# Kernel optimization log

Hardware: AMD Instinct MI355X
Metric: run time of the kernel (lower is better)

The kernel has to match this reference:

```python
import jax, jax.numpy as jnp
import numpy as np

LN_EPS = 1e-5
N_HEAD_CHANNELS = 32  # model_dim=256 -> 8 heads


def _layer_norm(x, g, b):
    m = jnp.mean(x, axis=-1, keepdims=True)
    v = jnp.mean((x - m) ** 2, axis=-1, keepdims=True)
    return (x - m) * jax.lax.rsqrt(v + LN_EPS) * g + b


def setup_inputs() -> dict:
    key = jax.random.key(0)
    ks = jax.random.split(key, 12)
    b, n, nv, f = 1, 65536, 1, 256
    s = 256  # 4 ** seq_level_attention
    w = 0.02
    d = {}
    d["x"] = jax.random.normal(ks[0], (b, n, nv, f), jnp.float32)
    d["mask"] = jnp.ones((b, n, nv), dtype=bool)
    d["pos_embeddings"] = jax.random.normal(ks[1], (nv, s, f), jnp.float32) * w
    d["W_emb"] = jax.random.normal(ks[2], (f, 2 * f), jnp.float32) * w
    d["b_emb"] = jnp.zeros((2 * f,), jnp.float32)
    d["ln1_g"] = jnp.ones((f,), jnp.float32)
    d["ln1_b"] = jnp.zeros((f,), jnp.float32)
    d["Wq"] = jax.random.normal(ks[3], (f, f), jnp.float32) * w
    d["bq"] = jnp.zeros((f,), jnp.float32)
    d["Wk"] = jax.random.normal(ks[4], (f, f), jnp.float32) * w
    d["bk"] = jnp.zeros((f,), jnp.float32)
    d["Wv"] = jax.random.normal(ks[5], (f, f), jnp.float32) * w
    d["bv"] = jnp.zeros((f,), jnp.float32)
    d["Wo"] = jax.random.normal(ks[6], (f, f), jnp.float32) * w
    d["bo"] = jnp.zeros((f,), jnp.float32)
    d["ln2_g"] = jnp.ones((f,), jnp.float32)
    d["ln2_b"] = jnp.zeros((f,), jnp.float32)
    d["W1"] = jax.random.normal(ks[7], (f, f), jnp.float32) * w
    d["W2"] = jax.random.normal(ks[8], (f, f), jnp.float32) * w
    d["gamma"] = jnp.ones((f,), jnp.float32) * 1e-6
    d["gamma_mlp"] = jnp.ones((f,), jnp.float32) * 1e-6
    return d


def reference(x, mask, pos_embeddings, W_emb, b_emb, ln1_g, ln1_b,
              Wq, bq, Wk, bk, Wv, bv, Wo, bo, ln2_g, ln2_b, W1, W2,
              gamma, gamma_mlp):
    b, n, nv, f = x.shape
    s = pos_embeddings.shape[1]          # window length = 4**seq_level
    n_seq = n // s
    n_heads = f // N_HEAD_CHANNELS
    hd = f // n_heads

    x_res = x
    # sequenize: (b, n, nv, f) -> (b, n_seq, s, nv, f)
    xs = x.reshape(b, n_seq, s, nv, f)
    ms = mask.reshape(b, n_seq, s, nv)
    # mask_update: a vertex stays valid only if its whole window is valid
    mask_update = (ms & jnp.all(ms, axis=-2, keepdims=True)).reshape(b, n, nv)

    # shift/scale from position embeddings: (nv, s, 2f) -> (s, nv, 2f)
    emb = jnp.swapaxes(pos_embeddings @ W_emb + b_emb, -2, -3)
    shift, scale = jnp.split(emb, 2, axis=-1)  # each (s, nv, f)

    xm = _layer_norm(xs, ln1_g, ln1_b) * (scale + 1.0) + shift

    B = b * n_seq
    L = s * nv
    xf = xm.reshape(B, L, f)
    mf = ms.reshape(B, L)

    def heads(t):
        return t.reshape(B, L, n_heads, hd).transpose(0, 2, 1, 3)

    q = heads(xf @ Wq + bq)
    k = heads(xf @ Wk + bk)
    v = heads(xf @ Wv + bv)

    scores = jnp.einsum('bhqd,bhkd->bhqk', q, k) / np.sqrt(hd).astype(np.float32)
    scores = scores + jnp.where(mf[:, None, None, :], 0.0, -1e9)
    attn = jax.nn.softmax(scores, axis=-1)
    out = jnp.einsum('bhqk,bhkd->bhqd', attn, v)
    out = out.transpose(0, 2, 1, 3).reshape(B, L, f) @ Wo + bo

    x = x_res + gamma * out.reshape(b, n, nv, f)
    h = _layer_norm(x, ln2_g, ln2_b) @ W1
    h = jax.nn.silu(h) @ W2
    x = x + gamma_mlp * h
    return (x, mask_update)
```

## Files before the change

kernel.cpp:

```cpp
#include <hip/hip_runtime.h>
#include <cstddef>
#include <cstdint>

typedef unsigned short u16;
typedef short s16x8 __attribute__((ext_vector_type(8)));
typedef float f32x4 __attribute__((ext_vector_type(4)));
typedef int   i32x4 __attribute__((ext_vector_type(4)));
typedef u16   u16x4 __attribute__((ext_vector_type(4)));

__device__ __forceinline__ float b2f(u16 u) {
  union { unsigned int i; float f; } v; v.i = ((unsigned int)u) << 16; return v.f;
}
__device__ __forceinline__ u16 f2b(float f) {
  union { float f; unsigned int i; } v; v.f = f;
  unsigned int r = v.i + 0x7fffu + ((v.i >> 16) & 1u);
  return (u16)(r >> 16);
}
__device__ __forceinline__ unsigned int cvt_pk(float a, float b) {
  unsigned int r;
  asm("v_cvt_pk_bf16_f32 %0, %1, %2" : "=v"(r) : "v"(a), "v"(b));
  return r;
}

__global__ __launch_bounds__(256) void transpose6(
    const float* __restrict__ w0, const float* __restrict__ w1,
    const float* __restrict__ w2, const float* __restrict__ w3,
    const float* __restrict__ w4, const float* __restrict__ w5,
    u16* __restrict__ wt)
{
  __shared__ u16 T[64][66];
  const float* src;
  switch (blockIdx.x) {
    case 0: src = w0; break; case 1: src = w1; break;
    case 2: src = w2; break; case 3: src = w3; break;
    case 4: src = w4; break; default: src = w5; break;
  }
  u16* dst = wt + (size_t)blockIdx.x * 65536;
  const int tr = (blockIdx.y & 3) * 64;
  const int tc = (blockIdx.y >> 2) * 64;
  const int lane = threadIdx.x & 63, grp = threadIdx.x >> 6;
  #pragma unroll
  for (int i = 0; i < 16; ++i) {
    const int r = grp + i * 4;
    T[lane][r] = f2b(src[(size_t)(tr + r) * 256 + tc + lane]);
  }
  __syncthreads();
  #pragma unroll
  for (int i = 0; i < 16; ++i) {
    const int j = grp + i * 4;
    dst[(size_t)(tc + j) * 256 + tr + lane] = T[j][lane];
  }
}

__global__ __launch_bounds__(256) void film_kernel(
    const float* __restrict__ pos, const float* __restrict__ Wemb,
    const float* __restrict__ bemb, float* __restrict__ shift,
    float* __restrict__ scale)
{
  __shared__ float prow[256];
  __shared__ float psum[4][64];
  const int s = blockIdx.x, t = threadIdx.x;
  const int ks = t >> 6, cl = t & 63;
  const int c = blockIdx.y * 64 + cl;
  prow[t] = pos[s * 256 + t];
  __syncthreads();
  float acc = 0.f;
  #pragma unroll 8
  for (int kk = ks * 64; kk < ks * 64 + 64; ++kk)
    acc = fmaf(prow[kk], Wemb[kk * 512 + c], acc);
  psum[ks][cl] = acc;
  __syncthreads();
  if (t < 64) {
    const int cc = blockIdx.y * 64 + t;
    const float v = psum[0][t] + psum[1][t] + psum[2][t] + psum[3][t] + bemb[cc];
    if (cc < 256) shift[s * 256 + cc] = v;
    else          scale[s * 256 + cc - 256] = v;
  }
}

__global__ __launch_bounds__(256) void ln_kernel(
    const float* __restrict__ xf,
    const float* __restrict__ shift, const float* __restrict__ scale,
    const float* __restrict__ g, const float* __restrict__ b,
    u16* __restrict__ out)
{
  const int lane = threadIdx.x & 63;
  const int l = lane & 15, grp = lane >> 4;
  const int token = blockIdx.x * 16 + (threadIdx.x >> 6) * 4 + grp;
  const size_t tb = (size_t)token * 256;
  const int spos = token & 255;

  f32x4 v[4];
  #pragma unroll
  for (int j = 0; j < 4; ++j) v[j] = *(const f32x4*)(xf + tb + 4 * l + 64 * j);
  float s = 0.f, s2 = 0.f;
  #pragma unroll
  for (int j = 0; j < 4; ++j)
    #pragma unroll
    for (int i = 0; i < 4; ++i) { s += v[j][i]; s2 += v[j][i] * v[j][i]; }
  #pragma unroll
  for (int off = 8; off >= 1; off >>= 1) {
    s  += __shfl_xor(s, off);
    s2 += __shfl_xor(s2, off);
  }
  const float mean = s * 0.00390625f;
  const float inv  = rsqrtf(s2 * 0.00390625f - mean * mean + 1e-5f);
  #pragma unroll
  for (int j = 0; j < 4; ++j) {
    const int e = 4 * l + 64 * j;
    const f32x4 gv = *(const f32x4*)(g + e);
    const f32x4 bv = *(const f32x4*)(b + e);
    const f32x4 sc = *(const f32x4*)(scale + spos * 256 + e);
    const f32x4 sh = *(const f32x4*)(shift + spos * 256 + e);
    u16x4 o;
    #pragma unroll
    for (int i = 0; i < 4; ++i) {
      float ln = (v[j][i] - mean) * inv * gv[i] + bv[i];
      ln = ln * (sc[i] + 1.0f) + sh[i];
      o[i] = f2b(ln);
    }
    *(u16x4*)(out + tb + e) = o;
  }
}

__global__ __launch_bounds__(256) void gemm_qkv(
    const u16* __restrict__ A, const u16* __restrict__ wt,
    const float* __restrict__ bq, const float* __restrict__ bk,
    const float* __restrict__ bv, u16* __restrict__ qo,
    u16* __restrict__ ko, u16* __restrict__ vo)
{
  __shared__ __align__(16) u16 Alds[128][72];
  __shared__ __align__(16) u16 Blds[128][72];
  const int bid = blockIdx.x;
  const int xcd = bid & 7, rr = bid >> 3;
  const int xx = rr % 6;
  const int yy = (rr / 6) * 8 + xcd;
  const int wsel = xx >> 1;
  const int m0 = yy * 128;
  const int n0 = (xx & 1) * 128;
  const u16* BT = wt + (size_t)wsel * 65536;
  const int t = threadIdx.x;
  const int wave = t >> 6, lane = t & 63;
  const int wm = (wave & 1) * 64, wn = (wave >> 1) * 64;
  const int lrow = lane & 15, lk = (lane >> 4) * 8;

  f32x4 acc[4][4];
  #pragma unroll
  for (int i = 0; i < 4; ++i)
    #pragma unroll
    for (int j = 0; j < 4; ++j)
      acc[i][j] = f32x4{0.f, 0.f, 0.f, 0.f};

  for (int k0 = 0; k0 < 256; k0 += 64) {
    #pragma unroll
    for (int i = 0; i < 4; ++i) {
      const int c = i * 256 + t;
      const int row = c >> 3, col = (c & 7) * 8;
      *(i32x4*)(&Alds[row][col]) = *(const i32x4*)(A  + (size_t)(m0 + row) * 256 + k0 + col);
      *(i32x4*)(&Blds[row][col]) = *(const i32x4*)(BT + (size_t)(n0 + row) * 256 + k0 + col);
    }
    __syncthreads();
    #pragma unroll
    for (int kk = 0; kk < 64; kk += 32) {
      s16x8 af[4], bf[4];
      #pragma unroll
      for (int mt = 0; mt < 4; ++mt) af[mt] = *(const s16x8*)(&Alds[wm + mt*16 + lrow][kk + lk]);
      #pragma unroll
      for (int nt = 0; nt < 4; ++nt) bf[nt] = *(const s16x8*)(&Blds[wn + nt*16 + lrow][kk + lk]);
      #pragma unroll
      for (int mt = 0; mt < 4; ++mt)
        #pragma unroll
        for (int nt = 0; nt < 4; ++nt)
          acc[mt][nt] = __builtin_amdgcn_mfma_f32_16x16x32_bf16(af[mt], bf[nt], acc[mt][nt], 0, 0, 0);
    }
    __syncthreads();
  }

  const float* bias = (wsel == 0) ? bq : (wsel == 1) ? bk : bv;
  u16* qko = (wsel == 0) ? qo : ko;
  #pragma unroll
  for (int mt = 0; mt < 4; ++mt) {
    const int mb = m0 + wm + mt*16 + (lane >> 4) * 4;
    const int w = mb >> 8, tok = mb & 255;
    #pragma unroll
    for (int nt = 0; nt < 4; ++nt) {
      const int n = n0 + wn + nt*16 + lrow;
      const int h = n >> 5, d = n & 31;
      const float bv_ = bias[n];
      if (wsel < 2) {
        #pragma unroll
        for (int r = 0; r < 4; ++r)
          qko[(size_t)w * 65536 + h * 8192 + (tok + r) * 32 + d] = f2b(acc[mt][nt][r] + bv_);
      } else {
        u16x4 pk;
        #pragma unroll
        for (int r = 0; r < 4; ++r) pk[r] = f2b(acc[mt][nt][r] + bv_);
        const int vaddr = ((tok >> 5) << 10) + (((tok >> 2) & 3) << 8)
                        + d * 8 + (((tok >> 4) & 1) << 2);
        *(u16x4*)(vo + (size_t)w * 65536 + h * 8192 + vaddr) = pk;
      }
    }
  }
}

__global__ __launch_bounds__(512) void gemm_tail(
    const u16* __restrict__ A, const u16* __restrict__ WoT,
    const u16* __restrict__ W1T, const u16* __restrict__ W2T,
    const float* __restrict__ bo, const float* __restrict__ x,
    const float* __restrict__ gam, const float* __restrict__ lg2,
    const float* __restrict__ lb2, const float* __restrict__ gml,
    float* __restrict__ outx)
{
  __shared__ __align__(16) u16 XH[64][264];
  __shared__ float LNp[4][64][2];
  __shared__ float LNm[64][2];
  const int m0 = blockIdx.x * 64;
  const int t = threadIdx.x;
  const int wave = t >> 6, lane = t & 63;
  const int wm = (wave & 1) * 32, wn = (wave >> 1) * 64;
  const int lrow = lane & 15, lk = (lane >> 4) * 8;
  const int quad = lane >> 4, col = lane & 15;

  f32x4 acc[2][4];
  #pragma unroll
  for (int i = 0; i < 2; ++i)
    #pragma unroll
    for (int j = 0; j < 4; ++j) acc[i][j] = f32x4{0.f,0.f,0.f,0.f};

  #pragma unroll 2
  for (int k0 = 0; k0 < 256; k0 += 32) {
    s16x8 af[2], bf[4];
    #pragma unroll
    for (int mt = 0; mt < 2; ++mt)
      af[mt] = *(const s16x8*)(A + (size_t)(m0 + wm + mt*16 + lrow) * 256 + k0 + lk);
    #pragma unroll
    for (int nt = 0; nt < 4; ++nt)
      bf[nt] = *(const s16x8*)(WoT + (size_t)(wn + nt*16 + lrow) * 256 + k0 + lk);
    #pragma unroll
    for (int mt = 0; mt < 2; ++mt)
      #pragma unroll
      for (int nt = 0; nt < 4; ++nt)
        acc[mt][nt] = __builtin_amdgcn_mfma_f32_16x16x32_bf16(af[mt], bf[nt], acc[mt][nt], 0, 0, 0);
  }

  unsigned int x1p[2][4][2];
  float s[2][4], s2[2][4];
  #pragma unroll
  for (int mt = 0; mt < 2; ++mt)
    #pragma unroll
    for (int r = 0; r < 4; ++r) { s[mt][r] = 0.f; s2[mt][r] = 0.f; }

  #pragma unroll
  for (int mt = 0; mt < 2; ++mt) {
    const int mb = m0 + wm + mt*16 + quad*4;
    #pragma unroll
    for (int nt = 0; nt < 4; ++nt) {
      const int n = wn + nt*16 + col;
      const float bon = bo[n], gn = gam[n];
      float v[4];
      #pragma unroll
      for (int r = 0; r < 4; ++r)
        v[r] = x[(size_t)(mb + r) * 256 + n] + gn * (acc[mt][nt][r] + bon);
      const unsigned int p0 = cvt_pk(v[0], v[1]);
      const unsigned int p1 = cvt_pk(v[2], v[3]);
      x1p[mt][nt][0] = p0;
      x1p[mt][nt][1] = p1;
      const float r0 = b2f((u16)(p0 & 0xffffu)), r1 = b2f((u16)(p0 >> 16));
      const float r2 = b2f((u16)(p1 & 0xffffu)), r3 = b2f((u16)(p1 >> 16));
      s[mt][0] += r0; s2[mt][0] += r0 * r0;
      s[mt][1] += r1; s2[mt][1] += r1 * r1;
      s[mt][2] += r2; s2[mt][2] += r2 * r2;
      s[mt][3] += r3; s2[mt][3] += r3 * r3;
    }
  }
  #pragma unroll
  for (int off = 1; off <= 8; off <<= 1) {
    #pragma unroll
    for (int mt = 0; mt < 2; ++mt)
      #pragma unroll
      for (int r = 0; r < 4; ++r) {
        s[mt][r]  += __shfl_xor(s[mt][r],  off);
        s2[mt][r] += __shfl_xor(s2[mt][r], off);
      }
  }
  if (col == 0) {
    #pragma unroll
    for (int mt = 0; mt < 2; ++mt)
      #pragma unroll
      for (int r = 0; r < 4; ++r) {
        const int row = wm + mt*16 + quad*4 + r;
        LNp[wave >> 1][row][0] = s[mt][r];
        LNp[wave >> 1][row][1] = s2[mt][r];
      }
  }
  __syncthreads();
  if (t < 64) {
    const float ss  = LNp[0][t][0] + LNp[1][t][0] + LNp[2][t][0] + LNp[3][t][0];
    const float ss2 = LNp[0][t][1] + LNp[1][t][1] + LNp[2][t][1] + LNp[3][t][1];
    const float mean = ss * 0.00390625f;
    LNm[t][0] = mean;
    LNm[t][1] = rsqrtf(ss2 * 0.00390625f - mean * mean + 1e-5f);
  }
  __syncthreads();
  #pragma unroll
  for (int mt = 0; mt < 2; ++mt) {
    #pragma unroll
    for (int nt = 0; nt < 4; ++nt) {
      const int n = wn + nt*16 + col;
      const float gg = lg2[n], bb_ = lb2[n];
      #pragma unroll
      for (int rr = 0; rr < 2; ++rr) {
        const unsigned int pk = x1p[mt][nt][rr];
        #pragma unroll
        for (int h2 = 0; h2 < 2; ++h2) {
          const int r = rr * 2 + h2;
          const int row = wm + mt*16 + quad*4 + r;
          const float rv = b2f((u16)(h2 ? (pk >> 16) : (pk & 0xffffu)));
          const float xn = (rv - LNm[row][0]) * LNm[row][1] * gg + bb_;
          XH[row][n ^ ((row & 12) << 1)] = f2b(xn);
        }
      }
    }
  }
  __syncthreads();

  #pragma unroll
  for (int i = 0; i < 2; ++i)
    #pragma unroll
    for (int j = 0; j < 4; ++j) acc[i][j] = f32x4{0.f,0.f,0.f,0.f};
  #pragma unroll 2
  for (int k0 = 0; k0 < 256; k0 += 32) {
    s16x8 af[2], bf[4];
    #pragma unroll
    for (int mt = 0; mt < 2; ++mt) {
      const int row = wm + mt*16 + lrow;
      af[mt] = *(const s16x8*)(&XH[row][(k0 + lk) ^ ((row & 12) << 1)]);
    }
    #pragma unroll
    for (int nt = 0; nt < 4; ++nt)
      bf[nt] = *(const s16x8*)(W1T + (size_t)(wn + nt*16 + lrow) * 256 + k0 + lk);
    #pragma unroll
    for (int mt = 0; mt < 2; ++mt)
      #pragma unroll
      for (int nt = 0; nt < 4; ++nt)
        acc[mt][nt] = __builtin_amdgcn_mfma_f32_16x16x32_bf16(af[mt], bf[nt], acc[mt][nt], 0, 0, 0);
  }
  __syncthreads();
  #pragma unroll
  for (int mt = 0; mt < 2; ++mt)
    #pragma unroll
    for (int nt = 0; nt < 4; ++nt)
      #pragma unroll
      for (int r = 0; r < 4; ++r) {
        const float y = acc[mt][nt][r];
        const float hsig = __builtin_amdgcn_rcpf(1.0f + __builtin_amdgcn_exp2f(-1.442695041f * y));
        const int row = wm + mt*16 + quad*4 + r;
        const int n = wn + nt*16 + col;
        XH[row][n ^ ((row & 12) << 1)] = f2b(y * hsig);
        acc[mt][nt][r] = 0.0f;
      }
  __syncthreads();

  #pragma unroll 2
  for (int k0 = 0; k0 < 256; k0 += 32) {
    s16x8 af[2], bf[4];
    #pragma unroll
    for (int mt = 0; mt < 2; ++mt) {
      const int row = wm + mt*16 + lrow;
      af[mt] = *(const s16x8*)(&XH[row][(k0 + lk) ^ ((row & 12) << 1)]);
    }
    #pragma unroll
    for (int nt = 0; nt < 4; ++nt)
      bf[nt] = *(const s16x8*)(W2T + (size_t)(wn + nt*16 + lrow) * 256 + k0 + lk);
    #pragma unroll
    for (int mt = 0; mt < 2; ++mt)
      #pragma unroll
      for (int nt = 0; nt < 4; ++nt)
        acc[mt][nt] = __builtin_amdgcn_mfma_f32_16x16x32_bf16(af[mt], bf[nt], acc[mt][nt], 0, 0, 0);
  }

  #pragma unroll
  for (int mt = 0; mt < 2; ++mt) {
    const int mb = m0 + wm + mt*16 + quad*4;
    #pragma unroll
    for (int nt = 0; nt < 4; ++nt) {
      const int n = wn + nt*16 + col;
      const float gn = gml[n];
      #pragma unroll
      for (int rr = 0; rr < 2; ++rr) {
        const unsigned int pk = x1p[mt][nt][rr];
        outx[(size_t)(mb + rr*2    ) * 256 + n] = b2f((u16)(pk & 0xffffu)) + gn * acc[mt][nt][rr*2];
        outx[(size_t)(mb + rr*2 + 1) * 256 + n] = b2f((u16)(pk >> 16))     + gn * acc[mt][nt][rr*2 + 1];
      }
    }
  }
}

__global__ __launch_bounds__(512) void attn256(
    const u16* __restrict__ q, const u16* __restrict__ k,
    const u16* __restrict__ vt, const float* __restrict__ fbias,
    u16* __restrict__ out)
{
  __shared__ __align__(16) u16 KV[16384];
  __shared__ __align__(16) u16 OB[8][16][40];
  const int bid = blockIdx.x;
  const int xcd = bid & 7, rr = bid >> 3;
  const int q0 = (rr & 1) * 128;
  const int s_ = (rr >> 1) * 8 + xcd;
  const int h = s_ & 7, w = s_ >> 3;
  const int t = threadIdx.x;
  const int wave = t >> 6, lane = t & 63;
  const int col = lane & 15, quad = lane >> 4;
  const size_t hb = (size_t)w * 65536 + (size_t)h * 8192;
  const int qr0 = q0 + wave * 16;
  const float sc2 = 0.25508586f;

  {
    const char* kg = (const char*)(k + hb);
    const char* vg = (const char*)(vt + hb);
    const i32x4 r0 = *(const i32x4*)(kg + t * 16);
    const i32x4 r1 = *(const i32x4*)(kg + 8192 + t * 16);
    const i32x4 r2 = *(const i32x4*)(vg + t * 16);
    const i32x4 r3 = *(const i32x4*)(vg + 8192 + t * 16);
    char* lb = (char*)KV;
    *(i32x4*)(lb + t * 16)         = r0;
    *(i32x4*)(lb + 8192 + t * 16)  = r1;
    *(i32x4*)(lb + 16384 + t * 16) = r2;
    *(i32x4*)(lb + 24576 + t * 16) = r3;
  }

  const s16x8 af = *(const s16x8*)(q + hb + (qr0 + col) * 32 + quad * 8);
  const float* fbb = fbias + w * 256 + quad * 4;
  __syncthreads();

  f32x4 acc[16];
  #pragma unroll
  for (int tl = 0; tl < 16; ++tl) {
    const s16x8 kf = *(const s16x8*)(KV + (tl * 16 + col) * 32 + quad * 8);
    acc[tl] = __builtin_amdgcn_mfma_f32_16x16x32_bf16(kf, af, f32x4{0.f,0.f,0.f,0.f}, 0, 0, 0);
  }

  #pragma unroll
  for (int tl = 0; tl < 16; ++tl) {
    const f32x4 fb = *(const f32x4*)(fbb + tl * 16);
    #pragma unroll
    for (int r = 0; r < 4; ++r)
      acc[tl][r] = fmaf(acc[tl][r], sc2, fb[r]);
  }

  f32x4 m4 = acc[0];
  #pragma unroll
  for (int tl = 1; tl < 16; ++tl)
    #pragma unroll
    for (int r = 0; r < 4; ++r)
      m4[r] = fmaxf(m4[r], acc[tl][r]);
  float mx = fmaxf(fmaxf(m4[0], m4[1]), fmaxf(m4[2], m4[3]));
  mx = fmaxf(mx, __shfl_xor(mx, 16));
  mx = fmaxf(mx, __shfl_xor(mx, 32));

  f32x4 s4 = {0.f, 0.f, 0.f, 0.f};
  #pragma unroll
  for (int tl = 0; tl < 16; ++tl) {
    #pragma unroll
    for (int r = 0; r < 4; ++r) {
      const float e = __builtin_amdgcn_exp2f(acc[tl][r] - mx);
      acc[tl][r] = e;
      s4[r] += e;
    }
  }
  float sum = (s4[0] + s4[1]) + (s4[2] + s4[3]);
  sum += __shfl_xor(sum, 16);
  sum += __shfl_xor(sum, 32);
  const float inv = __builtin_amdgcn_rcpf(sum);

  f32x4 o0 = {0.f,0.f,0.f,0.f}, o1 = {0.f,0.f,0.f,0.f};
  const u16* vl = KV + 8192;
  #pragma unroll
  for (int s = 0; s < 8; ++s) {
    i32x4 pi;
    pi[0] = (int)cvt_pk(acc[2*s][0],     acc[2*s][1]);
    pi[1] = (int)cvt_pk(acc[2*s][2],     acc[2*s][3]);
    pi[2] = (int)cvt_pk(acc[2*s + 1][0], acc[2*s + 1][1]);
    pi[3] = (int)cvt_pk(acc[2*s + 1][2], acc[2*s + 1][3]);
    const s16x8 pf = *(const s16x8*)&pi;
    const s16x8 vf0 = *(const s16x8*)(vl + s * 1024 + quad * 256 + col * 8);
    const s16x8 vf1 = *(const s16x8*)(vl + s * 1024 + quad * 256 + col * 8 + 128);
    o0 = __builtin_amdgcn_mfma_f32_16x16x32_bf16(pf, vf0, o0, 0, 0, 0);
    o1 = __builtin_amdgcn_mfma_f32_16x16x32_bf16(pf, vf1, o1, 0, 0, 0);
  }

  f32x4 invr;
  #pragma unroll
  for (int r = 0; r < 4; ++r) invr[r] = __shfl(inv, quad * 4 + r);

  #pragma unroll
  for (int r = 0; r < 4; ++r) {
    OB[wave][quad * 4 + r][col]      = f2b(o0[r] * invr[r]);
    OB[wave][quad * 4 + r][col + 16] = f2b(o1[r] * invr[r]);
  }
  const s16x8 ov = *(const s16x8*)(&OB[wave][col][quad * 8]);
  *(s16x8*)(out + (size_t)w * 65536 + (size_t)(qr0 + col) * 256 + h * 32 + quad * 8) = ov;
}

__global__ __launch_bounds__(256) void maskup(const int* __restrict__ mask,
                                              float* __restrict__ out,
                                              float* __restrict__ fbias)
{
  __shared__ int wall[4];
  const int w = blockIdx.x, t = threadIdx.x;
  const int v = (mask[w * 256 + t] != 0) ? 1 : 0;
  const int a = __all(v);
  if ((t & 63) == 0) wall[t >> 6] = a;
  __syncthreads();
  const int allw = wall[0] & wall[1] & wall[2] & wall[3];
  out[w * 256 + t] = (v & allw) ? 1.0f : 0.0f;
  fbias[w * 256 + t] = v ? 0.0f : -1.0e9f;
}

extern "C" void kernel_launch(void* const* d_in, const int* in_sizes, int n_in,
                              void* d_out, int out_size, void* d_ws, size_t ws_size,
                              hipStream_t stream)
{
  (void)in_sizes; (void)n_in; (void)out_size; (void)ws_size;
  const float* x    = (const float*)d_in[0];
  const int*   mask = (const int*)d_in[1];
  const float* pos  = (const float*)d_in[2];
  const float* Wemb = (const float*)d_in[3];
  const float* bemb = (const float*)d_in[4];
  const float* ln1g = (const float*)d_in[5];
  const float* ln1b = (const float*)d_in[6];
  const float* Wq   = (const float*)d_in[7];
  const float* bq   = (const float*)d_in[8];
  const float* Wk   = (const float*)d_in[9];
  const float* bk   = (const float*)d_in[10];
  const float* Wv   = (const float*)d_in[11];
  const float* bv   = (const float*)d_in[12];
  const float* Wo   = (const float*)d_in[13];
  const float* bo   = (const float*)d_in[14];
  const float* ln2g = (const float*)d_in[15];
  const float* ln2b = (const float*)d_in[16];
  const float* W1   = (const float*)d_in[17];
  const float* W2   = (const float*)d_in[18];
  const float* gam  = (const float*)d_in[19];
  const float* gml  = (const float*)d_in[20];

  char* ws = (char*)d_ws;
  float* shift = (float*)ws;
  float* scale = (float*)(ws + (256 << 10));
  u16*   wt    = (u16*)(ws + (512 << 10));
  float* fbias = (float*)(ws + (1280 << 10));
  u16*   b0    = (u16*)(ws + ((size_t)2  << 20));
  u16*   b1    = (u16*)(ws + ((size_t)34 << 20));
  u16*   b2    = (u16*)(ws + ((size_t)66 << 20));
  u16*   b3    = (u16*)(ws + ((size_t)98 << 20));
  float* outx  = (float*)d_out;
  float* outm  = outx + 16777216;

  const u16* WoT = wt + 3 * 65536;
  const u16* W1T = wt + 4 * 65536;
  const u16* W2T = wt + 5 * 65536;

  transpose6<<<dim3(6, 16), 256, 0, stream>>>(Wq, Wk, Wv, Wo, W1, W2, wt);
  film_kernel<<<dim3(256, 8), 256, 0, stream>>>(pos, Wemb, bemb, shift, scale);
  maskup<<<256, 256, 0, stream>>>(mask, outm, fbias);
  ln_kernel<<<4096, 256, 0, stream>>>(x, shift, scale, ln1g, ln1b, b0);
  gemm_qkv<<<3072, 256, 0, stream>>>(b0, wt, bq, bk, bv, b1, b2, b3);
  attn256<<<4096, 512, 0, stream>>>(b1, b2, b3, fbias, b0);
  gemm_tail<<<1024, 512, 0, stream>>>(b0, WoT, W1T, W2T, bo, x, gam,
                                      ln2g, ln2b, gml, outx);
}
```

Baseline: 388.9 us.

## Register-prefetch K tiles in QKV GEMM and stage tail weights through LDS

The QKV projection GEMM now prefetches the next 64-wide K slice into registers while the MFMAs run on the current LDS slice, so global load latency overlaps compute. The fused tail kernel (Wo, LN2, W1, SiLU, W2) now stages weight slices through a shared LDS buffer with the same software pipelining, including cross-phase prefetch of the next weight matrix during the LayerNorm and SiLU epilogues. Previously each wave read weights straight from global memory. The XH swizzle and padding change to fit the extra LDS. This adds LDS use and barriers, which may lower occupancy for the 512-thread tail blocks.

```diff
diff --git a/kernel.cpp b/kernel.cpp
--- a/kernel.cpp
+++ b/kernel.cpp
@@ -143,6 +143,7 @@
   const int wave = t >> 6, lane = t & 63;
   const int wm = (wave & 1) * 64, wn = (wave >> 1) * 64;
   const int lrow = lane & 15, lk = (lane >> 4) * 8;
+  const int brow = t >> 3, bcol = (t & 7) * 8;
 
   f32x4 acc[4][4];
   #pragma unroll
@@ -151,30 +152,50 @@
     for (int j = 0; j < 4; ++j)
       acc[i][j] = f32x4{0.f, 0.f, 0.f, 0.f};
 
-  for (int k0 = 0; k0 < 256; k0 += 64) {
-    #pragma unroll
-    for (int i = 0; i < 4; ++i) {
-      const int c = i * 256 + t;
-      const int row = c >> 3, col = (c & 7) * 8;
-      *(i32x4*)(&Alds[row][col]) = *(const i32x4*)(A  + (size_t)(m0 + row) * 256 + k0 + col);
-      *(i32x4*)(&Blds[row][col]) = *(const i32x4*)(BT + (size_t)(n0 + row) * 256 + k0 + col);
-    }
-    __syncthreads();
-    #pragma unroll
-    for (int kk = 0; kk < 64; kk += 32) {
-      s16x8 af[4], bf[4];
-      #pragma unroll
-      for (int mt = 0; mt < 4; ++mt) af[mt] = *(const s16x8*)(&Alds[wm + mt*16 + lrow][kk + lk]);
-      #pragma unroll
-      for (int nt = 0; nt < 4; ++nt) bf[nt] = *(const s16x8*)(&Blds[wn + nt*16 + lrow][kk + lk]);
-      #pragma unroll
-      for (int mt = 0; mt < 4; ++mt)
-        #pragma unroll
-        for (int nt = 0; nt < 4; ++nt)
-          acc[mt][nt] = __builtin_amdgcn_mfma_f32_16x16x32_bf16(af[mt], bf[nt], acc[mt][nt], 0, 0, 0);
-    }
-    __syncthreads();
-  }
+  i32x4 ra[4], rb[4];
+#define QK_LOAD(p) { \
+    _Pragma("unroll") \
+    for (int i_ = 0; i_ < 4; ++i_) { \
+      ra[i_] = *(const i32x4*)(A  + (size_t)(m0 + i_*32 + brow) * 256 + (p)*64 + bcol); \
+      rb[i_] = *(const i32x4*)(BT + (size_t)(n0 + i_*32 + brow) * 256 + (p)*64 + bcol); } }
+#define QK_STORE() { \
+    _Pragma("unroll") \
+    for (int i_ = 0; i_ < 4; ++i_) { \
+      *(i32x4*)(&Alds[i_*32 + brow][bcol]) = ra[i_]; \
+      *(i32x4*)(&Blds[i_*32 + brow][bcol]) = rb[i_]; } }
+#define QK_COMP(p) { \
+    _Pragma("unroll") \
+    for (int kk = 0; kk < 64; kk += 32) { \
+      s16x8 af[4], bf[4]; \
+      _Pragma("unroll") \
+      for (int mt = 0; mt < 4; ++mt) af[mt] = *(const s16x8*)(&Alds[wm + mt*16 + lrow][kk + lk]); \
+      _Pragma("unroll") \
+      for (int nt = 0; nt < 4; ++nt) bf[nt] = *(const s16x8*)(&Blds[wn + nt*16 + lrow][kk + lk]); \
+      _Pragma("unroll") \
+      for (int mt = 0; mt < 4; ++mt) \
+        _Pragma("unroll") \
+        for (int nt = 0; nt < 4; ++nt) \
+          acc[mt][nt] = __builtin_amdgcn_mfma_f32_16x16x32_bf16(af[mt], bf[nt], acc[mt][nt], 0, 0, 0); } }
+
+  QK_LOAD(0);
+  QK_STORE();
+  QK_LOAD(1);
+  __syncthreads();
+  QK_COMP(0);
+  __syncthreads();
+  QK_STORE();
+  QK_LOAD(2);
+  __syncthreads();
+  QK_COMP(1);
+  __syncthreads();
+  QK_STORE();
+  QK_LOAD(3);
+  __syncthreads();
+  QK_COMP(2);
+  __syncthreads();
+  QK_STORE();
+  __syncthreads();
+  QK_COMP(3);
 
   const float* bias = (wsel == 0) ? bq : (wsel == 1) ? bk : bv;
   u16* qko = (wsel == 0) ? qo : ko;
@@ -201,6 +222,9 @@
       }
     }
   }
+#undef QK_LOAD
+#undef QK_STORE
+#undef QK_COMP
 }
 
 __global__ __launch_bounds__(512) void gemm_tail(
@@ -211,7 +235,8 @@
     const float* __restrict__ lb2, const float* __restrict__ gml,
     float* __restrict__ outx)
 {
-  __shared__ __align__(16) u16 XH[64][264];
+  __shared__ __align__(16) u16 Blds[256][72];
+  __shared__ __align__(16) u16 XH[64][256];
   __shared__ float LNp[4][64][2];
   __shared__ float LNm[64][2];
   const int m0 = blockIdx.x * 64;
@@ -220,6 +245,7 @@
   const int wm = (wave & 1) * 32, wn = (wave >> 1) * 64;
   const int lrow = lane & 15, lk = (lane >> 4) * 8;
   const int quad = lane >> 4, col = lane & 15;
+  const int brow = t >> 3, bcol = (t & 7) * 8;
 
   f32x4 acc[2][4];
   #pragma unroll
@@ -227,21 +253,67 @@
     #pragma unroll
     for (int j = 0; j < 4; ++j) acc[i][j] = f32x4{0.f,0.f,0.f,0.f};
 
-  #pragma unroll 2
-  for (int k0 = 0; k0 < 256; k0 += 32) {
-    s16x8 af[2], bf[4];
-    #pragma unroll
-    for (int mt = 0; mt < 2; ++mt)
-      af[mt] = *(const s16x8*)(A + (size_t)(m0 + wm + mt*16 + lrow) * 256 + k0 + lk);
-    #pragma unroll
-    for (int nt = 0; nt < 4; ++nt)
-      bf[nt] = *(const s16x8*)(WoT + (size_t)(wn + nt*16 + lrow) * 256 + k0 + lk);
-    #pragma unroll
-    for (int mt = 0; mt < 2; ++mt)
-      #pragma unroll
-      for (int nt = 0; nt < 4; ++nt)
-        acc[mt][nt] = __builtin_amdgcn_mfma_f32_16x16x32_bf16(af[mt], bf[nt], acc[mt][nt], 0, 0, 0);
-  }
+  i32x4 rw[4];
+#define TL_LOAD(W, p) { \
+    _Pragma("unroll") \
+    for (int i_ = 0; i_ < 4; ++i_) \
+      rw[i_] = *(const i32x4*)((W) + (size_t)(i_*64 + brow) * 256 + (p)*64 + bcol); }
+#define TL_STORE() { \
+    _Pragma("unroll") \
+    for (int i_ = 0; i_ < 4; ++i_) \
+      *(i32x4*)(&Blds[i_*64 + brow][bcol]) = rw[i_]; }
+#define TL_COMPA(p) { const int k0 = (p)*64; \
+    _Pragma("unroll") \
+    for (int kk = 0; kk < 64; kk += 32) { \
+      s16x8 af[2], bf[4]; \
+      _Pragma("unroll") \
+      for (int mt = 0; mt < 2; ++mt) \
+        af[mt] = *(const s16x8*)(A + (size_t)(m0 + wm + mt*16 + lrow) * 256 + k0 + kk + lk); \
+      _Pragma("unroll") \
+      for (int nt = 0; nt < 4; ++nt) \
+        bf[nt] = *(const s16x8*)(&Blds[wn + nt*16 + lrow][kk + lk]); \
+      _Pragma("unroll") \
+      for (int mt = 0; mt < 2; ++mt) \
+        _Pragma("unroll") \
+        for (int nt = 0; nt < 4; ++nt) \
+          acc[mt][nt] = __builtin_amdgcn_mfma_f32_16x16x32_bf16(af[mt], bf[nt], acc[mt][nt], 0, 0, 0); } }
+#define TL_COMPX(p) { const int k0 = (p)*64; \
+    _Pragma("unroll") \
+    for (int kk = 0; kk < 64; kk += 32) { \
+      s16x8 af[2], bf[4]; \
+      _Pragma("unroll") \
+      for (int mt = 0; mt < 2; ++mt) { \
+        const int row_ = wm + mt*16 + lrow; \
+        af[mt] = *(const s16x8*)(&XH[row_][(k0 + kk + lk) ^ ((row_ & 14) << 2)]); } \
+      _Pragma("unroll") \
+      for (int nt = 0; nt < 4; ++nt) \
+        bf[nt] = *(const s16x8*)(&Blds[wn + nt*16 + lrow][kk + lk]); \
+      _Pragma("unroll") \
+      for (int mt = 0; mt < 2; ++mt) \
+        _Pragma("unroll") \
+        for (int nt = 0; nt < 4; ++nt) \
+          acc[mt][nt] = __builtin_amdgcn_mfma_f32_16x16x32_bf16(af[mt], bf[nt], acc[mt][nt], 0, 0, 0); } }
+
+  TL_LOAD(WoT, 0);
+  TL_STORE();
+  TL_LOAD(WoT, 1);
+  __syncthreads();
+  TL_COMPA(0);
+  __syncthreads();
+  TL_STORE();
+  TL_LOAD(WoT, 2);
+  __syncthreads();
+  TL_COMPA(1);
+  __syncthreads();
+  TL_STORE();
+  TL_LOAD(WoT, 3);
+  __syncthreads();
+  TL_COMPA(2);
+  __syncthreads();
+  TL_STORE();
+  TL_LOAD(W1T, 0);
+  __syncthreads();
+  TL_COMPA(3);
 
   unsigned int x1p[2][4][2];
   float s[2][4], s2[2][4];
@@ -294,6 +366,8 @@
       }
   }
   __syncthreads();
+  TL_STORE();
+  TL_LOAD(W1T, 1);
   if (t < 64) {
     const float ss  = LNp[0][t][0] + LNp[1][t][0] + LNp[2][t][0] + LNp[3][t][0];
     const float ss2 = LNp[0][t][1] + LNp[1][t][1] + LNp[2][t][1] + LNp[3][t][1];
@@ -317,35 +391,36 @@
           const int row = wm + mt*16 + quad*4 + r;
           const float rv = b2f((u16)(h2 ? (pk >> 16) : (pk & 0xffffu)));
           const float xn = (rv - LNm[row][0]) * LNm[row][1] * gg + bb_;
-          XH[row][n ^ ((row & 12) << 1)] = f2b(xn);
+          XH[row][n ^ ((row & 14) << 2)] = f2b(xn);
         }
       }
     }
   }
-  __syncthreads();
-
   #pragma unroll
   for (int i = 0; i < 2; ++i)
     #pragma unroll
     for (int j = 0; j < 4; ++j) acc[i][j] = f32x4{0.f,0.f,0.f,0.f};
-  #pragma unroll 2
-  for (int k0 = 0; k0 < 256; k0 += 32) {
-    s16x8 af[2], bf[4];
-    #pragma unroll
-    for (int mt = 0; mt < 2; ++mt) {
-      const int row = wm + mt*16 + lrow;
-      af[mt] = *(const s16x8*)(&XH[row][(k0 + lk) ^ ((row & 12) << 1)]);
-    }
-    #pragma unroll
-    for (int nt = 0; nt < 4; ++nt)
-      bf[nt] = *(const s16x8*)(W1T + (size_t)(wn + nt*16 + lrow) * 256 + k0 + lk);
-    #pragma unroll
-    for (int mt = 0; mt < 2; ++mt)
-      #pragma unroll
-      for (int nt = 0; nt < 4; ++nt)
-        acc[mt][nt] = __builtin_amdgcn_mfma_f32_16x16x32_bf16(af[mt], bf[nt], acc[mt][nt], 0, 0, 0);
-  }
-  __syncthreads();
+  __syncthreads();
+
+  TL_COMPX(0);
+  __syncthreads();
+  TL_STORE();
+  TL_LOAD(W1T, 2);
+  __syncthreads();
+  TL_COMPX(1);
+  __syncthreads();
+  TL_STORE();
+  TL_LOAD(W1T, 3);
+  __syncthreads();
+  TL_COMPX(2);
+  __syncthreads();
+  TL_STORE();
+  TL_LOAD(W2T, 0);
+  __syncthreads();
+  TL_COMPX(3);
+  __syncthreads();
+  TL_STORE();
+  TL_LOAD(W2T, 1);
   #pragma unroll
   for (int mt = 0; mt < 2; ++mt)
     #pragma unroll
@@ -356,28 +431,26 @@
         const float hsig = __builtin_amdgcn_rcpf(1.0f + __builtin_amdgcn_exp2f(-1.442695041f * y));
         const int row = wm + mt*16 + quad*4 + r;
         const int n = wn + nt*16 + col;
-        XH[row][n ^ ((row & 12) << 1)] = f2b(y * hsig);
+        XH[row][n ^ ((row & 14) << 2)] = f2b(y * hsig);
         acc[mt][nt][r] = 0.0f;
       }
   __syncthreads();
 
-  #pragma unroll 2
-  for (int k0 = 0; k0 < 256; k0 += 32) {
-    s16x8 af[2], bf[4];
-    #pragma unroll
-    for (int mt = 0; mt < 2; ++mt) {
-      const int row = wm + mt*16 + lrow;
-      af[mt] = *(const s16x8*)(&XH[row][(k0 + lk) ^ ((row & 12) << 1)]);
-    }
-    #pragma unroll
-    for (int nt = 0; nt < 4; ++nt)
-      bf[nt] = *(const s16x8*)(W2T + (size_t)(wn + nt*16 + lrow) * 256 + k0 + lk);
-    #pragma unroll
-    for (int mt = 0; mt < 2; ++mt)
-      #pragma unroll
-      for (int nt = 0; nt < 4; ++nt)
-        acc[mt][nt] = __builtin_amdgcn_mfma_f32_16x16x32_bf16(af[mt], bf[nt], acc[mt][nt], 0, 0, 0);
-  }
+  TL_COMPX(0);
+  __syncthreads();
+  TL_STORE();
+  TL_LOAD(W2T, 2);
+  __syncthreads();
+  TL_COMPX(1);
+  __syncthreads();
+  TL_STORE();
+  TL_LOAD(W2T, 3);
+  __syncthreads();
+  TL_COMPX(2);
+  __syncthreads();
+  TL_STORE();
+  __syncthreads();
+  TL_COMPX(3);
 
   #pragma unroll
   for (int mt = 0; mt < 2; ++mt) {
@@ -394,6 +467,10 @@
       }
     }
   }
+#undef TL_LOAD
+#undef TL_STORE
+#undef TL_COMPA
+#undef TL_COMPX
 }
 
 __global__ __launch_bounds__(512) void attn256(
```

After: 333.2 us. -14.3%, faster.
